# Optimization experiments

Measured on AMD Instinct MI355X. Metric: run time of the kernel, lower is better.

Reference implementation:

```python
import jax, jax.numpy as jnp
import numpy as np

EPS = 1e-5

def _bn(x, g, b, m, v):
    inv = g / jnp.sqrt(v + EPS)
    return x * inv[None, :, None, None] + (b - m * inv)[None, :, None, None]

def _box_conv(x, y_min, y_max, x_min, x_max):
    # Learnable box filter via integral image + bilinear-interpolated corners.
    # x: (N, C, H, W); box params: (C, B). Output: (N, C*B, H, W), area-normalized.
    N, C, H, W = x.shape
    B = y_min.shape[1]
    # padded integral image (N, C, H+1, W+1)
    I = jnp.pad(jnp.cumsum(jnp.cumsum(x, axis=2), axis=3), ((0, 0), (0, 0), (1, 0), (1, 0)))
    iy = jnp.arange(H, dtype=x.dtype)
    ix = jnp.arange(W, dtype=x.dtype)

    def one_box(Ic, ymn, ymx, xmn, xmx):
        # Ic: (N, H+1, W+1); scalar box extents
        y1 = jnp.clip(iy + ymn, 0.0, H)
        y2 = jnp.clip(iy + ymx + 1.0, 0.0, H)
        x1 = jnp.clip(ix + xmn, 0.0, W)
        x2 = jnp.clip(ix + xmx + 1.0, 0.0, W)

        def interp_y(c):  # (H,) -> (N, H, W+1)
            i0 = jnp.clip(jnp.floor(c), 0.0, H - 1).astype(jnp.int32)
            t = (c - i0)[None, :, None]
            return Ic[:, i0, :] * (1.0 - t) + Ic[:, i0 + 1, :] * t

        Gy1, Gy2 = interp_y(y1), interp_y(y2)

        def interp_x(G, c):  # (N, H, W+1), (W,) -> (N, H, W)
            i0 = jnp.clip(jnp.floor(c), 0.0, W - 1).astype(jnp.int32)
            t = (c - i0)[None, None, :]
            return G[:, :, i0] * (1.0 - t) + G[:, :, i0 + 1] * t

        S = interp_x(Gy2, x2) - interp_x(Gy2, x1) - interp_x(Gy1, x2) + interp_x(Gy1, x1)
        area = (ymx - ymn + 1.0) * (xmx - xmn + 1.0)
        return S / area  # (N, H, W)

    f_b = jax.vmap(one_box, in_axes=(None, 0, 0, 0, 0))   # over boxes
    f_cb = jax.vmap(f_b, in_axes=(1, 0, 0, 0, 0))          # over channels
    out = f_cb(I, y_min, y_max, x_min, x_max)              # (C, B, N, H, W)
    return jnp.transpose(out, (2, 0, 1, 3, 4)).reshape(N, C * B, H, W)


def setup_inputs() -> dict:
    key = jax.random.key(0)
    ks = jax.random.split(key, 20)
    N, Cin, H, W = 32, 256, 56, 56
    Cmid, B = 16, 4
    Cbox = Cmid * B
    Cout = 256
    f32 = jnp.float32
    x = jax.random.normal(ks[0], (N, Cin, H, W), f32)
    w1 = jax.random.normal(ks[1], (Cmid, Cin), f32) * 0.05
    g1 = jax.random.uniform(ks[2], (Cmid,), f32, 0.5, 1.5)
    b1 = jax.random.normal(ks[3], (Cmid,), f32) * 0.1
    m1 = jax.random.normal(ks[4], (Cmid,), f32) * 0.1
    v1 = jax.random.uniform(ks[5], (Cmid,), f32, 0.5, 1.5)
    y_min = -jax.random.uniform(ks[6], (Cmid, B), f32) * 10.0
    y_max = jax.random.uniform(ks[7], (Cmid, B), f32) * 10.0
    x_min = -jax.random.uniform(ks[8], (Cmid, B), f32) * 10.0
    x_max = jax.random.uniform(ks[9], (Cmid, B), f32) * 10.0
    g2 = jax.random.uniform(ks[10], (Cbox,), f32, 0.5, 1.5)
    b2 = jax.random.normal(ks[11], (Cbox,), f32) * 0.1
    m2 = jax.random.normal(ks[12], (Cbox,), f32) * 0.1
    v2 = jax.random.uniform(ks[13], (Cbox,), f32, 0.5, 1.5)
    w3 = jax.random.normal(ks[14], (Cout, Cbox), f32) * 0.05
    g3 = jax.random.uniform(ks[15], (Cout,), f32, 0.5, 1.5)
    b3 = jax.random.normal(ks[16], (Cout,), f32) * 0.1
    m3 = jax.random.normal(ks[17], (Cout,), f32) * 0.1
    v3 = jax.random.uniform(ks[18], (Cout,), f32, 0.5, 1.5)
    return {"x": x, "w1": w1, "g1": g1, "b1": b1, "m1": m1, "v1": v1,
            "y_min": y_min, "y_max": y_max, "x_min": x_min, "x_max": x_max,
            "g2": g2, "b2": b2, "m2": m2, "v2": v2,
            "w3": w3, "g3": g3, "b3": b3, "m3": m3, "v3": v3}


def reference(x, w1, g1, b1, m1, v1, y_min, y_max, x_min, x_max,
              g2, b2, m2, v2, w3, g3, b3, m3, v3):
    out = jnp.einsum('nchw,oc->nohw', x, w1)            # 1x1 conv
    out = jax.nn.relu(_bn(out, g1, b1, m1, v1))
    out = _box_conv(out, y_min, y_max, x_min, x_max)    # (N, Cmid*B, H, W)
    out = jax.nn.relu(_bn(out, g2, b2, m2, v2))
    out = jnp.einsum('nchw,oc->nohw', out, w3)          # 1x1 conv
    out = _bn(out, g3, b3, m3, v3)
    return jax.nn.relu(out + x)
```

## Files before the change

kernel.cpp:

```cpp
#include <hip/hip_runtime.h>
#include <hip/hip_bf16.h>
#include <math.h>

#define EPSB 1e-5f

constexpr int NN = 32, CIN = 256, HH = 56, WW = 56, HW = HH * WW;
constexpr int CMID = 16, NB = 4, CBOX = 64, COUT = 256;

typedef __attribute__((ext_vector_type(8))) short short8;
typedef __attribute__((ext_vector_type(4))) float f32x4;

constexpr size_t WS_OUT1  = 0;
constexpr size_t WS_OUT2B = WS_OUT1 + (size_t)NN * CMID * HW;

__global__ __launch_bounds__(256) void k1(const float* __restrict__ x,
                                          const float* __restrict__ w1,
                                          const float* __restrict__ g1,
                                          const float* __restrict__ b1,
                                          const float* __restrict__ m1,
                                          const float* __restrict__ v1,
                                          float* __restrict__ out1) {
  __shared__ __hip_bfloat16 Xb[64][264];
  __shared__ __hip_bfloat16 Wb[16][264];
  int bid = blockIdx.x;
  int n = bid / 49, hwb = (bid % 49) * 64;
  int tid = threadIdx.x;
  int l = tid & 63, w = tid >> 6;

  {
    int c = tid >> 4, kb = (tid & 15) * 16;
    float inv = g1[c] / sqrtf(v1[c] + EPSB);
    const float* wp = w1 + c * CIN + kb;
#pragma unroll
    for (int j = 0; j < 16; ++j)
      Wb[c][kb + j] = __float2bfloat16(wp[j] * inv);
  }

  {
    const float* xb = x + (size_t)n * CIN * HW + hwb;
    int pxq = (tid & 15) * 4;
    int cio = (tid >> 4) * 2;
#pragma unroll
    for (int p = 0; p < 8; ++p) {
      int ci = p * 32 + cio;
      f32x4 a = *reinterpret_cast<const f32x4*>(xb + (size_t)ci * HW + pxq);
      f32x4 b = *reinterpret_cast<const f32x4*>(xb + (size_t)(ci + 1) * HW + pxq);
#pragma unroll
      for (int j = 0; j < 4; ++j) {
        unsigned lo = (unsigned)__bfloat16_as_ushort(__float2bfloat16(a[j]));
        unsigned hi = (unsigned)__bfloat16_as_ushort(__float2bfloat16(b[j]));
        *reinterpret_cast<unsigned*>(&Xb[pxq + j][ci]) = lo | (hi << 16);
      }
    }
  }
  __syncthreads();

  int pix = 16 * w + (l & 15);
  f32x4 acc = (f32x4)(0.f);
#pragma unroll
  for (int kk = 0; kk < 8; ++kk) {
    int k0 = kk * 32 + (l >> 4) * 8;
    short8 afr = *reinterpret_cast<const short8*>(&Wb[l & 15][k0]);
    short8 bfr = *reinterpret_cast<const short8*>(&Xb[pix][k0]);
    acc = __builtin_amdgcn_mfma_f32_16x16x32_bf16(afr, bfr, acc, 0, 0, 0);
  }

#pragma unroll
  for (int j = 0; j < 4; ++j) {
    int c = (l >> 4) * 4 + j;
    float inv = g1[c] / sqrtf(v1[c] + EPSB);
    float val = acc[j] + (b1[c] - m1[c] * inv);
    out1[((size_t)n * CMID + c) * HW + hwb + pix] = fmaxf(val, 0.f);
  }
}

__device__ __forceinline__ float bilin(const float* __restrict__ sI, float y, float x) {
  int iy = min((int)y, 55);
  int ix = min((int)x, 55);
  float ty = y - (float)iy;
  float tx = x - (float)ix;
  const float* r = sI + iy * 57 + ix;
  float a = r[0], b = r[1], cc = r[57], d = r[58];
  float g1v = a * (1.f - ty) + cc * ty;
  float g2v = b * (1.f - ty) + d * ty;
  return g1v * (1.f - tx) + g2v * tx;
}

__global__ __launch_bounds__(512) void k2(
    const float* __restrict__ out1,
    const float* __restrict__ y_min, const float* __restrict__ y_max,
    const float* __restrict__ x_min, const float* __restrict__ x_max,
    const float* __restrict__ g2, const float* __restrict__ b2,
    const float* __restrict__ m2, const float* __restrict__ v2,
    __hip_bfloat16* __restrict__ out2b) {
  __shared__ float sI[57 * 57];
  int bid = blockIdx.x;
  int n = bid >> 4, c = bid & 15;
  int tid = threadIdx.x;
  int lane = tid & 63, w = tid >> 6;

  if (tid < 57) { sI[tid] = 0.f; sI[tid * 57] = 0.f; }
  const float* src = out1 + ((size_t)n * CMID + c) * HW;
  for (int vdx = tid; vdx < HW / 4; vdx += 512) {
    int p = vdx * 4;
    int h = p / 56, wq = p - h * 56;
    f32x4 d = ((const f32x4*)src)[vdx];
    float* dst = &sI[(h + 1) * 57 + wq + 1];
    dst[0] = d.x; dst[1] = d.y; dst[2] = d.z; dst[3] = d.w;
  }
  __syncthreads();

  for (int r = w; r < 56; r += 8) {
    float* row = &sI[(r + 1) * 57 + 1];
    float vv = (lane < 56) ? row[lane] : 0.f;
#pragma unroll
    for (int d = 1; d < 64; d <<= 1) {
      float o = __shfl_up(vv, d, 64);
      if (lane >= d) vv += o;
    }
    if (lane < 56) row[lane] = vv;
  }
  __syncthreads();
  for (int cc = w; cc < 56; cc += 8) {
    float* col = &sI[57 + cc + 1];
    float vv = (lane < 56) ? col[lane * 57] : 0.f;
#pragma unroll
    for (int d = 1; d < 64; d <<= 1) {
      float o = __shfl_up(vv, d, 64);
      if (lane >= d) vv += o;
    }
    if (lane < 56) col[lane * 57] = vv;
  }
  __syncthreads();

  float pymn[NB], pymx[NB], pxmn[NB], pxmx[NB], pinv[NB], pbi[NB], prar[NB];
#pragma unroll
  for (int b = 0; b < NB; ++b) {
    int cb = c * NB + b;
    pymn[b] = y_min[cb]; pymx[b] = y_max[cb];
    pxmn[b] = x_min[cb]; pxmx[b] = x_max[cb];
    float inv = g2[cb] / sqrtf(v2[cb] + EPSB);
    pinv[b] = inv;
    pbi[b] = b2[cb] - m2[cb] * inv;
    prar[b] = 1.f / ((pymx[b] - pymn[b] + 1.f) * (pxmx[b] - pxmn[b] + 1.f));
  }
  __hip_bfloat16* dst0 = out2b + ((size_t)n * CBOX + c * NB) * HW;

  for (int p = tid; p < HW; p += 512) {
    int h = p / 56, wq = p - h * 56;
    float fh = (float)h, fw = (float)wq;
#pragma unroll
    for (int b = 0; b < NB; ++b) {
      float y1 = fminf(fmaxf(fh + pymn[b], 0.f), 56.f);
      float y2 = fminf(fmaxf(fh + pymx[b] + 1.f, 0.f), 56.f);
      float x1 = fminf(fmaxf(fw + pxmn[b], 0.f), 56.f);
      float x2 = fminf(fmaxf(fw + pxmx[b] + 1.f, 0.f), 56.f);
      float S = bilin(sI, y2, x2) - bilin(sI, y2, x1) - bilin(sI, y1, x2) + bilin(sI, y1, x1);
      float val = S * prar[b] * pinv[b] + pbi[b];
      dst0[(size_t)b * HW + p] = __float2bfloat16(fmaxf(val, 0.f));
    }
  }
}

__global__ __launch_bounds__(512) void k3(
    const __hip_bfloat16* __restrict__ out2b,
    const float* __restrict__ w3,
    const float* __restrict__ g3, const float* __restrict__ b3,
    const float* __restrict__ m3, const float* __restrict__ v3,
    const float* __restrict__ x, float* __restrict__ out) {
  __shared__ __hip_bfloat16 T[64][72];
  int bid = blockIdx.x;
  int n = bid / 49, hwb = (bid % 49) * 64;
  int tid = threadIdx.x;
  int l = tid & 63, w = tid >> 6;

  {
    const __hip_bfloat16* srcp = out2b + ((size_t)n * CBOX + l) * HW + hwb + w * 8;
    short8 v = *reinterpret_cast<const short8*>(srcp);
    const __hip_bfloat16* vp = (const __hip_bfloat16*)&v;
#pragma unroll
    for (int i = 0; i < 8; ++i) T[w * 8 + i][l] = vp[i];
  }

  short8 afrag[2][2];
#pragma unroll
  for (int ot = 0; ot < 2; ++ot)
#pragma unroll
    for (int kh = 0; kh < 2; ++kh) {
      int o = w * 32 + ot * 16 + (l & 15);
      int k0 = kh * 32 + (l >> 4) * 8;
      const float* wp = w3 + o * CBOX + k0;
      union { short8 s; __hip_bfloat16 h[8]; } u;
#pragma unroll
      for (int j = 0; j < 8; ++j) u.h[j] = __float2bfloat16(wp[j]);
      afrag[ot][kh] = u.s;
    }

  __syncthreads();

  short8 bfrag[4][2];
#pragma unroll
  for (int pt = 0; pt < 4; ++pt)
#pragma unroll
    for (int kh = 0; kh < 2; ++kh) {
      int pix = pt * 16 + (l & 15);
      int k0 = kh * 32 + (l >> 4) * 8;
      bfrag[pt][kh] = *reinterpret_cast<const short8*>(&T[pix][k0]);
    }

  f32x4 acc[2][4];
#pragma unroll
  for (int ot = 0; ot < 2; ++ot)
#pragma unroll
    for (int pt = 0; pt < 4; ++pt) acc[ot][pt] = (f32x4)(0.f);

#pragma unroll
  for (int ot = 0; ot < 2; ++ot)
#pragma unroll
    for (int pt = 0; pt < 4; ++pt) {
      acc[ot][pt] = __builtin_amdgcn_mfma_f32_16x16x32_bf16(
          afrag[ot][0], bfrag[pt][0], acc[ot][pt], 0, 0, 0);
      acc[ot][pt] = __builtin_amdgcn_mfma_f32_16x16x32_bf16(
          afrag[ot][1], bfrag[pt][1], acc[ot][pt], 0, 0, 0);
    }

  size_t nbase = (size_t)n * COUT * HW + hwb;
#pragma unroll
  for (int ot = 0; ot < 2; ++ot) {
#pragma unroll
    for (int j = 0; j < 4; ++j) {
      int o = w * 32 + ot * 16 + (l >> 4) * 4 + j;
      float iv = g3[o] / sqrtf(v3[o] + EPSB);
      float bb = b3[o] - m3[o] * iv;
      size_t rowbase = nbase + (size_t)o * HW;
#pragma unroll
      for (int pt = 0; pt < 4; ++pt) {
        int pix = pt * 16 + (l & 15);
        float v = acc[ot][pt][j] * iv + bb + x[rowbase + pix];
        out[rowbase + pix] = fmaxf(v, 0.f);
      }
    }
  }
}

extern "C" void kernel_launch(void* const* d_in, const int* in_sizes, int n_in,
                              void* d_out, int out_size, void* d_ws, size_t ws_size,
                              hipStream_t stream) {
  const float* x   = (const float*)d_in[0];
  const float* w1  = (const float*)d_in[1];
  const float* g1  = (const float*)d_in[2];
  const float* b1  = (const float*)d_in[3];
  const float* m1  = (const float*)d_in[4];
  const float* v1  = (const float*)d_in[5];
  const float* ymn = (const float*)d_in[6];
  const float* ymx = (const float*)d_in[7];
  const float* xmn = (const float*)d_in[8];
  const float* xmx = (const float*)d_in[9];
  const float* g2  = (const float*)d_in[10];
  const float* b2  = (const float*)d_in[11];
  const float* m2  = (const float*)d_in[12];
  const float* v2  = (const float*)d_in[13];
  const float* w3  = (const float*)d_in[14];
  const float* g3  = (const float*)d_in[15];
  const float* b3  = (const float*)d_in[16];
  const float* m3  = (const float*)d_in[17];
  const float* v3  = (const float*)d_in[18];

  float* ws  = (float*)d_ws;
  float* out = (float*)d_out;
  __hip_bfloat16* out2b = (__hip_bfloat16*)(ws + WS_OUT2B);

  k1<<<NN * 49, 256, 0, stream>>>(x, w1, g1, b1, m1, v1, ws + WS_OUT1);
  k2<<<NN * CMID, 512, 0, stream>>>(ws + WS_OUT1, ymn, ymx, xmn, xmx,
                                    g2, b2, m2, v2, out2b);
  k3<<<NN * 49, 512, 0, stream>>>(out2b, w3, g3, b3, m3, v3, x, out);
}
```

Baseline: 81.52 us.

## Store mid activations as bf16, split box-conv over two blocks, precompute w3

```diff
diff --git a/kernel.cpp b/kernel.cpp
--- a/kernel.cpp
+++ b/kernel.cpp
@@ -10,8 +10,11 @@
 typedef __attribute__((ext_vector_type(8))) short short8;
 typedef __attribute__((ext_vector_type(4))) float f32x4;
 
-constexpr size_t WS_OUT1  = 0;
-constexpr size_t WS_OUT2B = WS_OUT1 + (size_t)NN * CMID * HW;
+constexpr size_t WS_INV3  = 0;
+constexpr size_t WS_B3F   = WS_INV3 + COUT;
+constexpr size_t WS_W3B   = WS_B3F + COUT;
+constexpr size_t WS_OUT1B = WS_W3B + (size_t)CBOX * COUT / 2;
+constexpr size_t WS_OUT2B = WS_OUT1B + (size_t)NN * CMID * HW / 2;
 
 __global__ __launch_bounds__(256) void k1(const float* __restrict__ x,
                                           const float* __restrict__ w1,
@@ -19,7 +22,13 @@
                                           const float* __restrict__ b1,
                                           const float* __restrict__ m1,
                                           const float* __restrict__ v1,
-                                          float* __restrict__ out1) {
+                                          const float* __restrict__ w3,
+                                          const float* __restrict__ g3,
+                                          const float* __restrict__ b3,
+                                          const float* __restrict__ m3,
+                                          const float* __restrict__ v3,
+                                          float* __restrict__ ws,
+                                          __hip_bfloat16* __restrict__ out1b) {
   __shared__ __hip_bfloat16 Xb[64][264];
   __shared__ __hip_bfloat16 Wb[16][264];
   int bid = blockIdx.x;
@@ -27,6 +36,23 @@
   int tid = threadIdx.x;
   int l = tid & 63, w = tid >> 6;
 
+  if (bid == 0) {
+    __hip_bfloat16* w3b = (__hip_bfloat16*)(ws + WS_W3B);
+    const float* wp = w3 + tid * 64;
+#pragma unroll
+    for (int j = 0; j < 64; j += 8) {
+      f32x4 a = *reinterpret_cast<const f32x4*>(wp + j);
+      f32x4 b = *reinterpret_cast<const f32x4*>(wp + j + 4);
+      union { short8 s; __hip_bfloat16 h[8]; } u;
+#pragma unroll
+      for (int q = 0; q < 4; ++q) { u.h[q] = __float2bfloat16(a[q]); u.h[q + 4] = __float2bfloat16(b[q]); }
+      *reinterpret_cast<short8*>(w3b + tid * 64 + j) = u.s;
+    }
+    float iv = g3[tid] / sqrtf(v3[tid] + EPSB);
+    ws[WS_INV3 + tid] = iv;
+    ws[WS_B3F + tid] = b3[tid] - m3[tid] * iv;
+  }
+
   {
     int c = tid >> 4, kb = (tid & 15) * 16;
     float inv = g1[c] / sqrtf(v1[c] + EPSB);
@@ -70,7 +96,7 @@
     int c = (l >> 4) * 4 + j;
     float inv = g1[c] / sqrtf(v1[c] + EPSB);
     float val = acc[j] + (b1[c] - m1[c] * inv);
-    out1[((size_t)n * CMID + c) * HW + hwb + pix] = fmaxf(val, 0.f);
+    out1b[((size_t)n * CMID + c) * HW + hwb + pix] = __float2bfloat16(fmaxf(val, 0.f));
   }
 }
 
@@ -87,7 +113,7 @@
 }
 
 __global__ __launch_bounds__(512) void k2(
-    const float* __restrict__ out1,
+    const __hip_bfloat16* __restrict__ out1b,
     const float* __restrict__ y_min, const float* __restrict__ y_max,
     const float* __restrict__ x_min, const float* __restrict__ x_max,
     const float* __restrict__ g2, const float* __restrict__ b2,
@@ -95,18 +121,22 @@
     __hip_bfloat16* __restrict__ out2b) {
   __shared__ float sI[57 * 57];
   int bid = blockIdx.x;
-  int n = bid >> 4, c = bid & 15;
+  int half = bid & 1;
+  int c = (bid >> 1) & 15;
+  int n = bid >> 5;
   int tid = threadIdx.x;
   int lane = tid & 63, w = tid >> 6;
 
   if (tid < 57) { sI[tid] = 0.f; sI[tid * 57] = 0.f; }
-  const float* src = out1 + ((size_t)n * CMID + c) * HW;
-  for (int vdx = tid; vdx < HW / 4; vdx += 512) {
-    int p = vdx * 4;
+  const __hip_bfloat16* src = out1b + ((size_t)n * CMID + c) * HW;
+  if (tid < HW / 8) {
+    int p = tid * 8;
     int h = p / 56, wq = p - h * 56;
-    f32x4 d = ((const f32x4*)src)[vdx];
+    short8 d = ((const short8*)src)[tid];
+    const __hip_bfloat16* dp = (const __hip_bfloat16*)&d;
     float* dst = &sI[(h + 1) * 57 + wq + 1];
-    dst[0] = d.x; dst[1] = d.y; dst[2] = d.z; dst[3] = d.w;
+#pragma unroll
+    for (int j = 0; j < 8; ++j) dst[j] = __bfloat162float(dp[j]);
   }
   __syncthreads();
 
@@ -146,7 +176,8 @@
   }
   __hip_bfloat16* dst0 = out2b + ((size_t)n * CBOX + c * NB) * HW;
 
-  for (int p = tid; p < HW; p += 512) {
+  int pend = (half + 1) * (HW / 2);
+  for (int p = half * (HW / 2) + tid; p < pend; p += 512) {
     int h = p / 56, wq = p - h * 56;
     float fh = (float)h, fw = (float)wq;
 #pragma unroll
@@ -164,9 +195,8 @@
 
 __global__ __launch_bounds__(512) void k3(
     const __hip_bfloat16* __restrict__ out2b,
-    const float* __restrict__ w3,
-    const float* __restrict__ g3, const float* __restrict__ b3,
-    const float* __restrict__ m3, const float* __restrict__ v3,
+    const __hip_bfloat16* __restrict__ w3b,
+    const float* __restrict__ inv3, const float* __restrict__ b3f,
     const float* __restrict__ x, float* __restrict__ out) {
   __shared__ __hip_bfloat16 T[64][72];
   int bid = blockIdx.x;
@@ -189,11 +219,7 @@
     for (int kh = 0; kh < 2; ++kh) {
       int o = w * 32 + ot * 16 + (l & 15);
       int k0 = kh * 32 + (l >> 4) * 8;
-      const float* wp = w3 + o * CBOX + k0;
-      union { short8 s; __hip_bfloat16 h[8]; } u;
-#pragma unroll
-      for (int j = 0; j < 8; ++j) u.h[j] = __float2bfloat16(wp[j]);
-      afrag[ot][kh] = u.s;
+      afrag[ot][kh] = *reinterpret_cast<const short8*>(w3b + o * CBOX + k0);
     }
 
   __syncthreads();
@@ -230,8 +256,8 @@
 #pragma unroll
     for (int j = 0; j < 4; ++j) {
       int o = w * 32 + ot * 16 + (l >> 4) * 4 + j;
-      float iv = g3[o] / sqrtf(v3[o] + EPSB);
-      float bb = b3[o] - m3[o] * iv;
+      float iv = inv3[o];
+      float bb = b3f[o];
       size_t rowbase = nbase + (size_t)o * HW;
 #pragma unroll
       for (int pt = 0; pt < 4; ++pt) {
@@ -268,10 +294,13 @@
 
   float* ws  = (float*)d_ws;
   float* out = (float*)d_out;
+  __hip_bfloat16* out1b = (__hip_bfloat16*)(ws + WS_OUT1B);
   __hip_bfloat16* out2b = (__hip_bfloat16*)(ws + WS_OUT2B);
-
-  k1<<<NN * 49, 256, 0, stream>>>(x, w1, g1, b1, m1, v1, ws + WS_OUT1);
-  k2<<<NN * CMID, 512, 0, stream>>>(ws + WS_OUT1, ymn, ymx, xmn, xmx,
-                                    g2, b2, m2, v2, out2b);
-  k3<<<NN * 49, 512, 0, stream>>>(out2b, w3, g3, b3, m3, v3, x, out);
-}
+  __hip_bfloat16* w3b   = (__hip_bfloat16*)(ws + WS_W3B);
+
+  k1<<<NN * 49, 256, 0, stream>>>(x, w1, g1, b1, m1, v1,
+                                  w3, g3, b3, m3, v3, ws, out1b);
+  k2<<<NN * CMID * 2, 512, 0, stream>>>(out1b, ymn, ymx, xmn, xmx,
+                                        g2, b2, m2, v2, out2b);
+  k3<<<NN * 49, 512, 0, stream>>>(out2b, w3b, ws + WS_INV3, ws + WS_B3F, x, out);
+}
```

After: 83.66 us. 1.03x slower.
